# Optimization experiments

Hardware: AMD Instinct MI355X
Metric: run time of the kernel (lower is better)

Reference implementation:

```python
import jax, jax.numpy as jnp
import numpy as np

DIM, E_DIM, HID = 512, 1024, 256
N_EXP, N_MIC, TOP_K, TOP_K_MIC = 8, 325, 2, 8
EPS_LN = 1e-5


def _layernorm(x, g, b):
    mu = x.mean(-1, keepdims=True)
    var = ((x - mu) ** 2).mean(-1, keepdims=True)
    return (x - mu) / jnp.sqrt(var + EPS_LN) * g + b


def setup_inputs() -> dict:
    key = jax.random.key(0)
    ks = jax.random.split(key, 20)
    s = 0.02
    return {
        "x": jax.random.normal(ks[0], (2, 512, DIM), jnp.float32),
        "router_w": jax.random.normal(ks[1], (N_EXP, DIM), jnp.float32) * s,
        "router_b": jnp.zeros((N_EXP,), jnp.float32),
        "exp_w1": jax.random.normal(ks[2], (N_EXP, E_DIM, DIM), jnp.float32) * s,
        "exp_b1": jnp.zeros((N_EXP, E_DIM), jnp.float32),
        "exp_w2": jax.random.normal(ks[3], (N_EXP, DIM, E_DIM), jnp.float32) * s,
        "exp_b2": jnp.zeros((N_EXP, DIM), jnp.float32),
        "mrouter_w": jax.random.normal(ks[4], (N_MIC, DIM), jnp.float32) * s,
        "mrouter_b": jnp.zeros((N_MIC,), jnp.float32),
        "mic_w1": jax.random.normal(ks[5], (N_MIC, HID, DIM), jnp.float32) * s,
        "mic_b1": jnp.zeros((N_MIC, HID), jnp.float32),
        "mic_w2": jax.random.normal(ks[6], (N_MIC, DIM, HID), jnp.float32) * s,
        "mic_b2": jnp.zeros((N_MIC, DIM), jnp.float32),
        "mic_g": jnp.ones((N_MIC, DIM), jnp.float32),
        "mic_beta": jnp.zeros((N_MIC, DIM), jnp.float32),
        "norm_g": jnp.ones((DIM,), jnp.float32),
        "norm_b": jnp.zeros((DIM,), jnp.float32),
    }


def _forward(x, router_w, router_b, exp_w1, exp_b1, exp_w2, exp_b2,
             mrouter_w, mrouter_b, mic_w1, mic_b1, mic_w2, mic_b2,
             mic_g, mic_beta, norm_g, norm_b):
    B, S, D = x.shape
    xf = x.reshape(-1, D)  # [T, D]

    # ---- expert routing (top-2 of 8) ----
    probs = jax.nn.softmax(xf @ router_w.T + router_b, axis=-1)
    topp, topi = jax.lax.top_k(probs, TOP_K)
    topp = topp / (topp.sum(-1, keepdims=True) + 1e-8)

    # dense compute over 8 experts, combine with top-k weights
    h = jax.nn.gelu(jnp.einsum('td,ehd->teh', xf, exp_w1) + exp_b1, approximate=False)
    ye = jnp.einsum('teh,edh->ted', h, exp_w2) + exp_b2  # [T, E, D]
    comb_w = (jax.nn.one_hot(topi, N_EXP, dtype=xf.dtype) * topp[..., None]).sum(1)  # [T, E]
    eo = jnp.einsum('te,ted->td', comb_w, ye)

    # ---- micro routing (top-8 of 325) ----
    mprobs = jax.nn.softmax(eo @ mrouter_w.T + mrouter_b, axis=-1)
    mtopp, mtopi = jax.lax.top_k(mprobs, TOP_K_MIC)
    mtopp = mtopp / (mtopp.sum(-1, keepdims=True) + 1e-8)

    def micro_slot(eo, p, idx):
        # gather per-token micro params, batched GEMV dispatch
        hm = jax.nn.gelu(jnp.einsum('td,thd->th', eo, mic_w1[idx]) + mic_b1[idx],
                         approximate=False)
        ym = jnp.einsum('th,tdh->td', hm, mic_w2[idx]) + mic_b2[idx]
        n = _layernorm(eo + ym, mic_g[idx], mic_beta[idx])
        return p[:, None] * n

    micro_slot = jax.checkpoint(micro_slot, static_argnums=())
    mo = jnp.zeros_like(eo)
    for k in range(TOP_K_MIC):  # small fixed loop over slots
        mo = mo + micro_slot(eo, mtopp[:, k], mtopi[:, k])

    combined = (eo + 0.1 * mo).reshape(B, S, D)
    return _layernorm(combined, norm_g, norm_b)


def reference(x, router_w, router_b, exp_w1, exp_b1, exp_w2, exp_b2,
              mrouter_w, mrouter_b, mic_w1, mic_b1, mic_w2, mic_b2,
              mic_g, mic_beta, norm_g, norm_b):
    return _forward(x, router_w, router_b, exp_w1, exp_b1, exp_w2, exp_b2,
                    mrouter_w, mrouter_b, mic_w1, mic_b1, mic_w2, mic_b2,
                    mic_g, mic_beta, norm_g, norm_b)
```

## Files before the change

### kernel.cpp

```cpp
#include <hip/hip_runtime.h>
#include <hip/hip_bf16.h>
#include <math.h>

#define T_TOK 1024
#define DIMM  512
#define EDIM  1024
#define HIDD  256
#define NEXP  8
#define NMIC  325
#define E16TILES 136
#define MTILES  840
#define NPAIR_M 8192

typedef __attribute__((ext_vector_type(8))) short bf16x8;
typedef __attribute__((ext_vector_type(8))) _Float16 f16x8;
typedef __attribute__((ext_vector_type(4))) float f32x4;

__device__ __forceinline__ float dot4(float4 a, float4 b) {
    return a.x*b.x + a.y*b.y + a.z*b.z + a.w*b.w;
}
__device__ __forceinline__ float gelu_exact(float x) {
    return 0.5f * x * (1.0f + erff(x * 0.70710678118654752f));
}
__device__ __forceinline__ float wave_sum(float v) {
    #pragma unroll
    for (int o = 32; o; o >>= 1) v += __shfl_xor(v, o);
    return v;
}
__device__ __forceinline__ short f2bf(float f) {
    union { __hip_bfloat16 h; short s; } u;
    u.h = __float2bfloat16(f);
    return u.s;
}
__device__ __forceinline__ short f2h(float f) {
    union { _Float16 h; short s; } u;
    u.h = (_Float16)f;
    return u.s;
}
__device__ __forceinline__ float h2f(short s) {
    union { _Float16 h; short s; } u;
    u.s = s;
    return (float)u.h;
}

__global__ void k_router(const float* __restrict__ x, const float* __restrict__ rw,
                         const float* __restrict__ rb, int* __restrict__ eidx,
                         float* __restrict__ ew, int* __restrict__ ecnt) {
    int wave = threadIdx.x >> 6, lane = threadIdx.x & 63;
    int t = blockIdx.x * 4 + wave;
    if (t >= T_TOK) return;
    const float* xr = x + (size_t)t * DIMM;
    float xv[8];
    #pragma unroll
    for (int j = 0; j < 8; ++j) xv[j] = xr[lane + 64*j];
    float p[NEXP];
    #pragma unroll
    for (int e = 0; e < NEXP; ++e) {
        const float* wr = rw + (size_t)e * DIMM;
        float a = 0.f;
        #pragma unroll
        for (int j = 0; j < 8; ++j) a += xv[j] * wr[lane + 64*j];
        p[e] = wave_sum(a) + rb[e];
    }
    float m = p[0];
    #pragma unroll
    for (int e = 1; e < NEXP; ++e) m = fmaxf(m, p[e]);
    float Z = 0.f;
    #pragma unroll
    for (int e = 0; e < NEXP; ++e) { p[e] = expf(p[e] - m); Z += p[e]; }
    #pragma unroll
    for (int e = 0; e < NEXP; ++e) p[e] /= Z;
    int i1 = 0; float v1 = p[0];
    #pragma unroll
    for (int e = 1; e < NEXP; ++e) if (p[e] > v1) { v1 = p[e]; i1 = e; }
    int i2 = -1; float v2 = -1.f;
    #pragma unroll
    for (int e = 0; e < NEXP; ++e) if (e != i1 && p[e] > v2) { v2 = p[e]; i2 = e; }
    float s = v1 + v2 + 1e-8f;
    if (lane == 0) {
        eidx[t*2] = i1; eidx[t*2+1] = i2;
        ew[t*2] = v1 / s; ew[t*2+1] = v2 / s;
        atomicAdd(&ecnt[i1], 1); atomicAdd(&ecnt[i2], 1);
    }
}

__global__ void k_scan(const int* __restrict__ cnt, int n, int pm,
                       int* __restrict__ off, int* __restrict__ cur,
                       int2* __restrict__ tiles, int* __restrict__ ntile) {
    __shared__ int s[512], s2[512];
    int tid = threadIdx.x;
    int v  = (tid < n) ? cnt[tid] : 0;
    int tc = (v + pm - 1) / pm;
    s[tid] = v; s2[tid] = tc;
    __syncthreads();
    for (int d = 1; d < 512; d <<= 1) {
        int a = (tid >= d) ? s[tid-d] : 0;
        int b = (tid >= d) ? s2[tid-d] : 0;
        __syncthreads();
        s[tid] += a; s2[tid] += b;
        __syncthreads();
    }
    int myoff = s[tid] - v, tb = s2[tid] - tc;
    if (tid < n) { off[tid] = myoff; cur[tid] = myoff; }
    if (tid == n-1) off[n] = s[tid];
    if (tid == 511) *ntile = s2[511];
    for (int j = 0; j < tc; ++j) tiles[tb + j] = make_int2(tid, myoff + j*pm);
}

__global__ void k_scatter(const int* __restrict__ idx, const float* __restrict__ w,
                          int total, int S, int* __restrict__ cur,
                          int* __restrict__ ptok, float* __restrict__ pw,
                          int* __restrict__ pmi) {
    int g = blockIdx.x * blockDim.x + threadIdx.x;
    if (g >= total) return;
    int t = g / S;
    int e = idx[g];
    int pos = atomicAdd(&cur[e], 1);
    ptok[pos] = t; pw[pos] = w[g]; pmi[pos] = e;
}

__global__ __launch_bounds__(256) void k_wsplit(const float* __restrict__ w,
                                                short* __restrict__ hi,
                                                short* __restrict__ lo, int n4) {
    int g = blockIdx.x * blockDim.x + threadIdx.x;
    if (g >= n4) return;
    float4 v = ((const float4*)w)[g];
    short4 h4, l4;
    h4.x = f2h(v.x); l4.x = f2h((v.x - h2f(h4.x)) * 4096.f);
    h4.y = f2h(v.y); l4.y = f2h((v.y - h2f(h4.y)) * 4096.f);
    h4.z = f2h(v.z); l4.z = f2h((v.z - h2f(h4.z)) * 4096.f);
    h4.w = f2h(v.w); l4.w = f2h((v.w - h2f(h4.w)) * 4096.f);
    ((short4*)hi)[g] = h4;
    ((short4*)lo)[g] = l4;
}

__global__ __launch_bounds__(256) void k_effn1(
    const float* __restrict__ x, const short* __restrict__ w1h, const short* __restrict__ w1l,
    const float* __restrict__ b1,
    const int2* __restrict__ tiles, const int* __restrict__ ntile,
    const int* __restrict__ eoff, const int* __restrict__ ep_tok,
    short* __restrict__ ghhi, short* __restrict__ ghlo) {
    if ((int)blockIdx.x >= *ntile) return;
    int2 tl = tiles[blockIdx.x];
    int e = tl.x, pbase = tl.y;
    int m = min(16, eoff[e+1] - pbase);
    int by = blockIdx.y;
    __shared__ __align__(16) short xh[8192];
    __shared__ __align__(16) short xl[8192];
    __shared__ int tok_s[16];
    int tid = threadIdx.x;
    if (tid < 16) tok_s[tid] = ep_tok[pbase + ((tid < m) ? tid : 0)];
    __syncthreads();
    int m0 = tid & 15;
    const float4* xrow = (const float4*)(x + (size_t)tok_s[m0] * DIMM);
    for (int kk = tid >> 4; kk < 128; kk += 16) {
        float4 v = xrow[kk];
        int off = ((kk >> 3) * 512) + ((((kk >> 1) & 3) * 16 + m0) * 8) + ((kk & 1) * 4);
        short4 h4, l4;
        h4.x = f2h(v.x); l4.x = f2h((v.x - h2f(h4.x)) * 4096.f);
        h4.y = f2h(v.y); l4.y = f2h((v.y - h2f(h4.y)) * 4096.f);
        h4.z = f2h(v.z); l4.z = f2h((v.z - h2f(h4.z)) * 4096.f);
        h4.w = f2h(v.w); l4.w = f2h((v.w - h2f(h4.w)) * 4096.f);
        *(short4*)(xh + off) = h4;
        *(short4*)(xl + off) = l4;
    }
    __syncthreads();
    int wave = tid >> 6, lane = tid & 63;
    int quad = lane >> 4, lcol = lane & 15;
    f32x4 zero = {0.f, 0.f, 0.f, 0.f};
    f32x4 acc0[8], acc1[8];
    #pragma unroll
    for (int q = 0; q < 8; ++q) { acc0[q] = zero; acc1[q] = zero; }
    const short* w1hb = w1h + (size_t)e * EDIM * DIMM;
    const short* w1lb = w1l + (size_t)e * EDIM * DIMM;
    for (int ks = 0; ks < 16; ++ks) {
        f16x8 ah = *(const f16x8*)(xh + ks*512 + lane*8);
        f16x8 al = *(const f16x8*)(xl + ks*512 + lane*8);
        int kb = ks*32 + quad*8;
        #pragma unroll
        for (int q = 0; q < 8; ++q) {
            int n = by*512 + wave*128 + q*16 + lcol;
            size_t wo = (size_t)n * DIMM + kb;
            f16x8 wh = *(const f16x8*)(w1hb + wo);
            f16x8 wl = *(const f16x8*)(w1lb + wo);
            acc0[q] = __builtin_amdgcn_mfma_f32_16x16x32_f16(ah, wh, acc0[q], 0, 0, 0);
            acc1[q] = __builtin_amdgcn_mfma_f32_16x16x32_f16(al, wh, acc1[q], 0, 0, 0);
            acc1[q] = __builtin_amdgcn_mfma_f32_16x16x32_f16(ah, wl, acc1[q], 0, 0, 0);
        }
    }
    __syncthreads();
    #pragma unroll
    for (int q = 0; q < 8; ++q) {
        int hp = wave*128 + q*16 + lcol;
        float bb = b1[(size_t)e * EDIM + by*512 + hp];
        int obase = ((hp >> 5) * 512) + (((hp >> 3) & 3) * 16) * 8 + (hp & 7);
        #pragma unroll
        for (int r = 0; r < 4; ++r) {
            int mm = quad*4 + r;
            float hv = gelu_exact(acc0[q][r] + acc1[q][r] * (1.f/4096.f) + bb);
            short hh = f2h(hv);
            xh[obase + mm*8] = hh;
            xl[obase + mm*8] = f2h((hv - h2f(hh)) * 4096.f);
        }
    }
    __syncthreads();
    short* dh = ghhi + (size_t)blockIdx.x * 16384 + (size_t)by * 8192;
    short* dl = ghlo + (size_t)blockIdx.x * 16384 + (size_t)by * 8192;
    const int4* sh = (const int4*)xh;
    const int4* sl = (const int4*)xl;
    #pragma unroll
    for (int j = 0; j < 4; ++j) {
        ((int4*)dh)[tid + 256*j] = sh[tid + 256*j];
        ((int4*)dl)[tid + 256*j] = sl[tid + 256*j];
    }
}

__global__ __launch_bounds__(256) void k_effn2(
    const short* __restrict__ ghhi, const short* __restrict__ ghlo,
    const short* __restrict__ w2h, const short* __restrict__ w2l, const float* __restrict__ b2,
    const int2* __restrict__ tiles, const int* __restrict__ ntile,
    const int* __restrict__ eoff, const int* __restrict__ ep_tok, const float* __restrict__ ep_w,
    float* __restrict__ eo) {
    if ((int)blockIdx.x >= *ntile) return;
    int2 tl = tiles[blockIdx.x];
    int e = tl.x, pbase = tl.y;
    int m = min(16, eoff[e+1] - pbase);
    int by = blockIdx.y;
    __shared__ int tok_s[16];
    __shared__ float pw_s[16];
    int tid = threadIdx.x;
    if (tid < 16) {
        int ok = tid < m;
        tok_s[tid] = ok ? ep_tok[pbase + tid] : 0;
        pw_s[tid]  = ok ? ep_w[pbase + tid] : 0.f;
    }
    __syncthreads();
    int wave = tid >> 6, lane = tid & 63;
    int quad = lane >> 4, lcol = lane & 15;
    const short* ahb = ghhi + (size_t)blockIdx.x * 16384;
    const short* alb = ghlo + (size_t)blockIdx.x * 16384;
    f32x4 zero = {0.f, 0.f, 0.f, 0.f};
    f32x4 acc0[4], acc1[4];
    #pragma unroll
    for (int q = 0; q < 4; ++q) { acc0[q] = zero; acc1[q] = zero; }
    const short* w2hb = w2h + (size_t)e * DIMM * EDIM;
    const short* w2lb = w2l + (size_t)e * DIMM * EDIM;
    for (int ks = 0; ks < 32; ++ks) {
        f16x8 ah = *(const f16x8*)(ahb + ks*512 + lane*8);
        f16x8 al = *(const f16x8*)(alb + ks*512 + lane*8);
        int kb = ks*32 + quad*8;
        #pragma unroll
        for (int q = 0; q < 4; ++q) {
            int d = by*256 + wave*64 + q*16 + lcol;
            size_t wo = (size_t)d * EDIM + kb;
            f16x8 wh = *(const f16x8*)(w2hb + wo);
            f16x8 wl = *(const f16x8*)(w2lb + wo);
            acc0[q] = __builtin_amdgcn_mfma_f32_16x16x32_f16(ah, wh, acc0[q], 0, 0, 0);
            acc1[q] = __builtin_amdgcn_mfma_f32_16x16x32_f16(al, wh, acc1[q], 0, 0, 0);
            acc1[q] = __builtin_amdgcn_mfma_f32_16x16x32_f16(ah, wl, acc1[q], 0, 0, 0);
        }
    }
    #pragma unroll
    for (int q = 0; q < 4; ++q) {
        int d = by*256 + wave*64 + q*16 + lcol;
        float bb = b2[(size_t)e * DIMM + d];
        #pragma unroll
        for (int r = 0; r < 4; ++r) {
            int mm = quad*4 + r;
            if (mm < m) {
                float val = (acc0[q][r] + acc1[q][r] * (1.f/4096.f) + bb) * pw_s[mm];
                atomicAdd(&eo[(size_t)tok_s[mm] * DIMM + d], val);
            }
        }
    }
}

__global__ __launch_bounds__(384) void k_mlog(
    const float* __restrict__ eo, const float* __restrict__ mw, const float* __restrict__ mb,
    float* __restrict__ mlog) {
    int t0 = blockIdx.x * 4;
    __shared__ float4 es[4][128];
    int tid = threadIdx.x;
    const float4* eo4 = (const float4*)eo;
    for (int q = tid; q < 4*128; q += 384) {
        int i = q >> 7, k = q & 127;
        es[i][k] = eo4[(size_t)(t0 + i) * 128 + k];
    }
    __syncthreads();
    if (tid < NMIC) {
        const float4* wr = (const float4*)(mw + (size_t)tid * DIMM);
        float acc[4] = {0.f, 0.f, 0.f, 0.f};
        for (int kk = 0; kk < 128; ++kk) {
            float4 wv = wr[kk];
            #pragma unroll
            for (int i = 0; i < 4; ++i) acc[i] += dot4(wv, es[i][kk]);
        }
        float bb = mb[tid];
        #pragma unroll
        for (int i = 0; i < 4; ++i) mlog[(size_t)(t0 + i) * NMIC + tid] = acc[i] + bb;
    }
}

__global__ void k_mtop(const float* __restrict__ mlog, int* __restrict__ mtopi,
                       float* __restrict__ mtopp, int* __restrict__ mcnt) {
    int wave = threadIdx.x >> 6, lane = threadIdx.x & 63;
    int t = blockIdx.x * 4 + wave;
    if (t >= T_TOK) return;
    float v[6]; int vi[6];
    #pragma unroll
    for (int j = 0; j < 6; ++j) {
        int n = lane + 64*j;
        vi[j] = n;
        v[j] = (n < NMIC) ? mlog[(size_t)t * NMIC + n] : -1e30f;
    }
    float M = v[0];
    #pragma unroll
    for (int j = 1; j < 6; ++j) M = fmaxf(M, v[j]);
    #pragma unroll
    for (int o = 32; o; o >>= 1) M = fmaxf(M, __shfl_xor(M, o));
    float Z = 0.f;
    #pragma unroll
    for (int j = 0; j < 6; ++j) Z += expf(v[j] - M);
    Z = wave_sum(Z);
    float bk[8]; int bi[8];
    for (int k = 0; k < 8; ++k) {
        float lv = v[0]; int li = vi[0];
        #pragma unroll
        for (int j = 1; j < 6; ++j)
            if (v[j] > lv) { lv = v[j]; li = vi[j]; }
        #pragma unroll
        for (int o = 32; o; o >>= 1) {
            float ov = __shfl_xor(lv, o); int oi = __shfl_xor(li, o);
            if (ov > lv || (ov == lv && oi < li)) { lv = ov; li = oi; }
        }
        bk[k] = expf(lv - M) / Z; bi[k] = li;
        #pragma unroll
        for (int j = 0; j < 6; ++j) if (vi[j] == li) v[j] = -1e30f;
    }
    float s = 0.f;
    #pragma unroll
    for (int k = 0; k < 8; ++k) s += bk[k];
    s += 1e-8f;
    if (lane == 0) {
        for (int k = 0; k < 8; ++k) {
            mtopi[t*8 + k] = bi[k];
            mtopp[t*8 + k] = bk[k] / s;
            atomicAdd(&mcnt[bi[k]], 1);
        }
    }
}

__global__ __launch_bounds__(256) void k_mffn1(
    const float* __restrict__ eo, const float* __restrict__ w1, const float* __restrict__ b1,
    const int2* __restrict__ tiles, const int* __restrict__ ntile,
    const int* __restrict__ moff, const int* __restrict__ mp_tok,
    short* __restrict__ ghbuf) {
    if ((int)blockIdx.x >= *ntile) return;
    int2 tl = tiles[blockIdx.x];
    int mi = tl.x, pbase = tl.y;
    int pm = min(16, moff[mi+1] - pbase);
    int by = blockIdx.y;
    __shared__ __align__(16) short eof[8192];
    __shared__ __align__(16) short hf[2048];
    __shared__ int tok_s[16];
    int tid = threadIdx.x;
    if (tid < 16) tok_s[tid] = mp_tok[pbase + ((tid < pm) ? tid : 0)];
    __syncthreads();
    int m0 = tid & 15;
    const float4* eorow = (const float4*)(eo + (size_t)tok_s[m0] * DIMM);
    for (int kk = tid >> 4; kk < 128; kk += 16) {
        float4 v = eorow[kk];
        int off = ((kk >> 3) * 512) + ((((kk >> 1) & 3) * 16 + m0) * 8) + ((kk & 1) * 4);
        short4 s4; s4.x = f2bf(v.x); s4.y = f2bf(v.y); s4.z = f2bf(v.z); s4.w = f2bf(v.w);
        *(short4*)(eof + off) = s4;
    }
    __syncthreads();
    int wave = tid >> 6, lane = tid & 63;
    int quad = lane >> 4, lcol = lane & 15;
    f32x4 zero = {0.f, 0.f, 0.f, 0.f};
    f32x4 accA[2];
    accA[0] = zero; accA[1] = zero;
    const float* w1base = w1 + (size_t)mi * HIDD * DIMM;
    for (int ks = 0; ks < 16; ++ks) {
        bf16x8 a = *(bf16x8*)(eof + ks*512 + lane*8);
        int kb = ks*32 + quad*8;
        #pragma unroll
        for (int q = 0; q < 2; ++q) {
            int n = by*128 + wave*32 + q*16 + lcol;
            const float* wp = w1base + (size_t)n * DIMM + kb;
            float4 wa = *(const float4*)wp;
            float4 wb = *(const float4*)(wp + 4);
            bf16x8 bfr;
            bfr[0]=f2bf(wa.x); bfr[1]=f2bf(wa.y); bfr[2]=f2bf(wa.z); bfr[3]=f2bf(wa.w);
            bfr[4]=f2bf(wb.x); bfr[5]=f2bf(wb.y); bfr[6]=f2bf(wb.z); bfr[7]=f2bf(wb.w);
            accA[q] = __builtin_amdgcn_mfma_f32_16x16x32_bf16(a, bfr, accA[q], 0, 0, 0);
        }
    }
    #pragma unroll
    for (int q = 0; q < 2; ++q) {
        int hp = wave*32 + q*16 + lcol;
        float bb = b1[(size_t)mi * HIDD + by*128 + hp];
        int obase = ((hp >> 5) * 512) + (((hp >> 3) & 3) * 16) * 8 + (hp & 7);
        #pragma unroll
        for (int r = 0; r < 4; ++r) {
            int mm = quad*4 + r;
            hf[obase + mm*8] = f2bf(gelu_exact(accA[q][r] + bb));
        }
    }
    __syncthreads();
    short* gh = ghbuf + (size_t)blockIdx.x * 4096 + (size_t)by * 2048;
    ((int4*)gh)[tid] = ((const int4*)hf)[tid];
}

__global__ __launch_bounds__(256) void k_mffn2(
    const short* __restrict__ ghbuf, const float* __restrict__ w2, const float* __restrict__ b2,
    const int2* __restrict__ tiles, const int* __restrict__ ntile, const int* __restrict__ moff,
    float* __restrict__ ybuf) {
    if ((int)blockIdx.x >= *ntile) return;
    int2 tl = tiles[blockIdx.x];
    int mi = tl.x, pbase = tl.y;
    int pm = min(16, moff[mi+1] - pbase);
    int by = blockIdx.y;
    int tid = threadIdx.x, wave = tid >> 6, lane = tid & 63;
    int quad = lane >> 4, lcol = lane & 15;
    const short* gh = ghbuf + (size_t)blockIdx.x * 4096;
    f32x4 zero = {0.f, 0.f, 0.f, 0.f};
    f32x4 accB[4];
    #pragma unroll
    for (int q = 0; q < 4; ++q) accB[q] = zero;
    const float* w2base = w2 + (size_t)mi * DIMM * HIDD;
    for (int ks = 0; ks < 8; ++ks) {
        bf16x8 a = *(const bf16x8*)(gh + ks*512 + lane*8);
        int kb = ks*32 + quad*8;
        #pragma unroll
        for (int q = 0; q < 4; ++q) {
            int d = by*256 + wave*64 + q*16 + lcol;
            const float* wp = w2base + (size_t)d * HIDD + kb;
            float4 wa = *(const float4*)wp;
            float4 wb = *(const float4*)(wp + 4);
            bf16x8 bfr;
            bfr[0]=f2bf(wa.x); bfr[1]=f2bf(wa.y); bfr[2]=f2bf(wa.z); bfr[3]=f2bf(wa.w);
            bfr[4]=f2bf(wb.x); bfr[5]=f2bf(wb.y); bfr[6]=f2bf(wb.z); bfr[7]=f2bf(wb.w);
            accB[q] = __builtin_amdgcn_mfma_f32_16x16x32_bf16(a, bfr, accB[q], 0, 0, 0);
        }
    }
    #pragma unroll
    for (int q = 0; q < 4; ++q) {
        int d = by*256 + wave*64 + q*16 + lcol;
        float bb = b2[(size_t)mi * DIMM + d];
        #pragma unroll
        for (int r = 0; r < 4; ++r) {
            int mm = quad*4 + r;
            if (mm < pm) ybuf[(size_t)(pbase + mm) * DIMM + d] = accB[q][r] + bb;
        }
    }
}

__global__ __launch_bounds__(256) void k_mln(
    const float* __restrict__ ybuf, const float* __restrict__ eo,
    const float* __restrict__ g, const float* __restrict__ beta,
    const int* __restrict__ mp_tok, const float* __restrict__ mp_w,
    const int* __restrict__ mp_mi, float* __restrict__ mo) {
    int wave = threadIdx.x >> 6, lane = threadIdx.x & 63;
    int p = blockIdx.x * 4 + wave;
    int t = mp_tok[p];
    int mi = mp_mi[p];
    float pw = mp_w[p];
    const float* yr = ybuf + (size_t)p * DIMM;
    const float* er = eo + (size_t)t * DIMM;
    float vv[8];
    float sum = 0.f;
    #pragma unroll
    for (int j = 0; j < 8; ++j) {
        int d = lane + 64*j;
        vv[j] = yr[d] + er[d];
        sum += vv[j];
    }
    sum = wave_sum(sum);
    float mu = sum * (1.f/512.f);
    float var = 0.f;
    #pragma unroll
    for (int j = 0; j < 8; ++j) { float d0 = vv[j] - mu; var += d0*d0; }
    var = wave_sum(var) * (1.f/512.f);
    float rstd = rsqrtf(var + 1e-5f);
    #pragma unroll
    for (int j = 0; j < 8; ++j) {
        int d = lane + 64*j;
        float nj = (vv[j] - mu) * rstd * g[(size_t)mi * DIMM + d] + beta[(size_t)mi * DIMM + d];
        atomicAdd(&mo[(size_t)t * DIMM + d], pw * nj);
    }
}

__global__ void k_final(const float* __restrict__ eo, const float* __restrict__ mo,
                        const float* __restrict__ g, const float* __restrict__ b,
                        float* __restrict__ out) {
    int wave = threadIdx.x >> 6, lane = threadIdx.x & 63;
    int t = blockIdx.x * 4 + wave;
    if (t >= T_TOK) return;
    float vv[8];
    float sum = 0.f;
    #pragma unroll
    for (int j = 0; j < 8; ++j) {
        int d = lane + 64*j;
        vv[j] = eo[(size_t)t * DIMM + d] + 0.1f * mo[(size_t)t * DIMM + d];
        sum += vv[j];
    }
    sum = wave_sum(sum);
    float mu = sum * (1.f/512.f);
    float var = 0.f;
    #pragma unroll
    for (int j = 0; j < 8; ++j) { float d0 = vv[j] - mu; var += d0*d0; }
    var = wave_sum(var) * (1.f/512.f);
    float rstd = rsqrtf(var + 1e-5f);
    #pragma unroll
    for (int j = 0; j < 8; ++j) {
        int d = lane + 64*j;
        out[(size_t)t * DIMM + d] = (vv[j] - mu) * rstd * g[d] + b[d];
    }
}

extern "C" void kernel_launch(void* const* d_in, const int* in_sizes, int n_in,
                              void* d_out, int out_size, void* d_ws, size_t ws_size,
                              hipStream_t stream) {
    const float* x    = (const float*)d_in[0];
    const float* rw   = (const float*)d_in[1];
    const float* rb   = (const float*)d_in[2];
    const float* ew1  = (const float*)d_in[3];
    const float* eb1  = (const float*)d_in[4];
    const float* ew2  = (const float*)d_in[5];
    const float* eb2  = (const float*)d_in[6];
    const float* mrw  = (const float*)d_in[7];
    const float* mrb  = (const float*)d_in[8];
    const float* mw1  = (const float*)d_in[9];
    const float* mb1  = (const float*)d_in[10];
    const float* mw2  = (const float*)d_in[11];
    const float* mb2  = (const float*)d_in[12];
    const float* mg   = (const float*)d_in[13];
    const float* mbeta= (const float*)d_in[14];
    const float* ng   = (const float*)d_in[15];
    const float* nb   = (const float*)d_in[16];
    float* out = (float*)d_out;

    char* w = (char*)d_ws;
    auto alloc = [&](size_t bytes) -> char* {
        char* p = w;
        w += (bytes + 255) & ~(size_t)255;
        return p;
    };
    const size_t WELEM = (size_t)NEXP * EDIM * DIMM;
    float* eo    = (float*)alloc((size_t)T_TOK * DIMM * 4);
    float* mo    = (float*)alloc((size_t)T_TOK * DIMM * 4);
    short* wspl  = (short*)alloc(WELEM * 2 * 4);
    short* w1h   = wspl;
    short* w1l   = wspl + WELEM;
    short* w2h   = wspl + 2*WELEM;
    short* w2l   = wspl + 3*WELEM;
    float* ybuf  = (float*)wspl;
    short* gfrag = (short*)alloc((size_t)E16TILES * 16384 * 2 * 2);
    short* ehhi  = gfrag;
    short* ehlo  = gfrag + (size_t)E16TILES * 16384;
    short* ghbuf = gfrag;
    float* mlog  = (float*)alloc((size_t)T_TOK * NMIC * 4);
    float* ewts  = (float*)alloc(2048 * 4);
    float* mtopp = (float*)alloc(8192 * 4);
    float* ep_w  = (float*)alloc(2048 * 4);
    float* mp_w  = (float*)alloc(8192 * 4);
    int*   eidx  = (int*)alloc(2048 * 4);
    int*   mtopi = (int*)alloc(8192 * 4);
    int*   cnts  = (int*)alloc((NEXP + NMIC) * 4);
    int*   ecnt  = cnts;
    int*   mcnt  = cnts + NEXP;
    int*   eoff  = (int*)alloc((NEXP + 1) * 4);
    int*   ecur  = (int*)alloc(NEXP * 4);
    int*   moff  = (int*)alloc((NMIC + 1) * 4);
    int*   mcur  = (int*)alloc(NMIC * 4);
    int2*  etile = (int2*)alloc(E16TILES * 8);
    int2*  mtile = (int2*)alloc(MTILES * 8);
    int*   entile= (int*)alloc(4);
    int*   mntile= (int*)alloc(4);
    int*   ep_tok= (int*)alloc(2048 * 4);
    int*   mp_tok= (int*)alloc(8192 * 4);
    int*   ep_mi = (int*)alloc(2048 * 4);
    int*   mp_mi = (int*)alloc(8192 * 4);

    hipMemsetAsync(eo, 0, (size_t)2 * T_TOK * DIMM * 4, stream);
    hipMemsetAsync(cnts, 0, (NEXP + NMIC) * 4, stream);

    int n4 = (int)(WELEM / 4);
    k_wsplit <<<n4/256, 256, 0, stream>>>(ew1, w1h, w1l, n4);
    k_wsplit <<<n4/256, 256, 0, stream>>>(ew2, w2h, w2l, n4);
    k_router <<<T_TOK/4, 256, 0, stream>>>(x, rw, rb, eidx, ewts, ecnt);
    k_scan   <<<1, 512, 0, stream>>>(ecnt, NEXP, 16, eoff, ecur, etile, entile);
    k_scatter<<<(T_TOK*2 + 255)/256, 256, 0, stream>>>(eidx, ewts, T_TOK*2, 2, ecur, ep_tok, ep_w, ep_mi);
    k_effn1  <<<dim3(E16TILES, 2, 1), 256, 0, stream>>>(x, w1h, w1l, eb1, etile, entile, eoff, ep_tok, ehhi, ehlo);
    k_effn2  <<<dim3(E16TILES, 2, 1), 256, 0, stream>>>(ehhi, ehlo, w2h, w2l, eb2, etile, entile, eoff, ep_tok, ep_w, eo);
    k_mlog   <<<T_TOK/4, 384, 0, stream>>>(eo, mrw, mrb, mlog);
    k_mtop   <<<T_TOK/4, 256, 0, stream>>>(mlog, mtopi, mtopp, mcnt);
    k_scan   <<<1, 512, 0, stream>>>(mcnt, NMIC, 16, moff, mcur, mtile, mntile);
    k_scatter<<<(T_TOK*8 + 255)/256, 256, 0, stream>>>(mtopi, mtopp, T_TOK*8, 8, mcur, mp_tok, mp_w, mp_mi);
    k_mffn1  <<<dim3(MTILES, 2, 1), 256, 0, stream>>>(eo, mw1, mb1, mtile, mntile, moff, mp_tok, ghbuf);
    k_mffn2  <<<dim3(MTILES, 2, 1), 256, 0, stream>>>(ghbuf, mw2, mb2, mtile, mntile, moff, ybuf);
    k_mln    <<<NPAIR_M/4, 256, 0, stream>>>(ybuf, eo, mg, mbeta, mp_tok, mp_w, mp_mi, mo);
    k_final  <<<T_TOK/4, 256, 0, stream>>>(eo, mo, ng, nb, out);
}
```

Baseline: 697.9 us.

## Pre-pack expert and micro-expert weights into MFMA fragment layout

```diff
diff --git a/kernel.cpp b/kernel.cpp
--- a/kernel.cpp
+++ b/kernel.cpp
@@ -41,6 +41,63 @@
     union { _Float16 h; short s; } u;
     u.s = s;
     return (float)u.h;
+}
+
+__global__ __launch_bounds__(256) void k_packbf(const float* __restrict__ src,
+                                                short* __restrict__ dst,
+                                                int K, int CK, int nchunk) {
+    int c = blockIdx.x;
+    int rt = c / nchunk, kc = c - rt * nchunk;
+    __shared__ __align__(16) short lds[8192];
+    int tid = threadIdx.x;
+    const float4* s4 = (const float4*)(src + (size_t)rt * 16 * K + (size_t)kc * CK);
+    int ck4 = CK >> 2;
+    int tot = 16 * ck4;
+    for (int q = tid; q < tot; q += 256) {
+        int i = q / ck4, kk = q - i * ck4;
+        float4 v = s4[(size_t)i * (K >> 2) + kk];
+        int off = ((kk >> 3) * 512) + ((((kk >> 1) & 3) * 16 + i) * 8) + ((kk & 1) * 4);
+        short4 b4; b4.x = f2bf(v.x); b4.y = f2bf(v.y); b4.z = f2bf(v.z); b4.w = f2bf(v.w);
+        *(short4*)(lds + off) = b4;
+    }
+    __syncthreads();
+    short* d = dst + (size_t)rt * 16 * K + (size_t)kc * 16 * CK;
+    int n16 = (16 * CK) >> 3;
+    for (int q = tid; q < n16; q += 256)
+        ((int4*)d)[q] = ((const int4*)lds)[q];
+}
+
+__global__ __launch_bounds__(256) void k_packhl(const float* __restrict__ src,
+                                                short* __restrict__ dsth,
+                                                short* __restrict__ dstl,
+                                                int K, int CK, int nchunk) {
+    int c = blockIdx.x;
+    int rt = c / nchunk, kc = c - rt * nchunk;
+    __shared__ __align__(16) short ldh[8192];
+    __shared__ __align__(16) short ldl[8192];
+    int tid = threadIdx.x;
+    const float4* s4 = (const float4*)(src + (size_t)rt * 16 * K + (size_t)kc * CK);
+    int ck4 = CK >> 2;
+    int tot = 16 * ck4;
+    for (int q = tid; q < tot; q += 256) {
+        int i = q / ck4, kk = q - i * ck4;
+        float4 v = s4[(size_t)i * (K >> 2) + kk];
+        int off = ((kk >> 3) * 512) + ((((kk >> 1) & 3) * 16 + i) * 8) + ((kk & 1) * 4);
+        short4 h4, l4;
+        h4.x = f2h(v.x); l4.x = f2h((v.x - h2f(h4.x)) * 4096.f);
+        h4.y = f2h(v.y); l4.y = f2h((v.y - h2f(h4.y)) * 4096.f);
+        h4.z = f2h(v.z); l4.z = f2h((v.z - h2f(h4.z)) * 4096.f);
+        h4.w = f2h(v.w); l4.w = f2h((v.w - h2f(h4.w)) * 4096.f);
+        *(short4*)(ldh + off) = h4;
+        *(short4*)(ldl + off) = l4;
+    }
+    __syncthreads();
+    size_t cb = (size_t)rt * 16 * K + (size_t)kc * 16 * CK;
+    int n16 = (16 * CK) >> 3;
+    for (int q = tid; q < n16; q += 256) {
+        ((int4*)(dsth + cb))[q] = ((const int4*)ldh)[q];
+        ((int4*)(dstl + cb))[q] = ((const int4*)ldl)[q];
+    }
 }
 
 __global__ void k_router(const float* __restrict__ x, const float* __restrict__ rw,
@@ -117,21 +174,6 @@
     int e = idx[g];
     int pos = atomicAdd(&cur[e], 1);
     ptok[pos] = t; pw[pos] = w[g]; pmi[pos] = e;
-}
-
-__global__ __launch_bounds__(256) void k_wsplit(const float* __restrict__ w,
-                                                short* __restrict__ hi,
-                                                short* __restrict__ lo, int n4) {
-    int g = blockIdx.x * blockDim.x + threadIdx.x;
-    if (g >= n4) return;
-    float4 v = ((const float4*)w)[g];
-    short4 h4, l4;
-    h4.x = f2h(v.x); l4.x = f2h((v.x - h2f(h4.x)) * 4096.f);
-    h4.y = f2h(v.y); l4.y = f2h((v.y - h2f(h4.y)) * 4096.f);
-    h4.z = f2h(v.z); l4.z = f2h((v.z - h2f(h4.z)) * 4096.f);
-    h4.w = f2h(v.w); l4.w = f2h((v.w - h2f(h4.w)) * 4096.f);
-    ((short4*)hi)[g] = h4;
-    ((short4*)lo)[g] = l4;
 }
 
 __global__ __launch_bounds__(256) void k_effn1(
@@ -171,18 +213,17 @@
     f32x4 acc0[8], acc1[8];
     #pragma unroll
     for (int q = 0; q < 8; ++q) { acc0[q] = zero; acc1[q] = zero; }
-    const short* w1hb = w1h + (size_t)e * EDIM * DIMM;
-    const short* w1lb = w1l + (size_t)e * EDIM * DIMM;
+    const short* whb = w1h + (size_t)e * EDIM * DIMM + (size_t)lane * 8;
+    const short* wlb = w1l + (size_t)e * EDIM * DIMM + (size_t)lane * 8;
     for (int ks = 0; ks < 16; ++ks) {
         f16x8 ah = *(const f16x8*)(xh + ks*512 + lane*8);
         f16x8 al = *(const f16x8*)(xl + ks*512 + lane*8);
-        int kb = ks*32 + quad*8;
         #pragma unroll
         for (int q = 0; q < 8; ++q) {
-            int n = by*512 + wave*128 + q*16 + lcol;
-            size_t wo = (size_t)n * DIMM + kb;
-            f16x8 wh = *(const f16x8*)(w1hb + wo);
-            f16x8 wl = *(const f16x8*)(w1lb + wo);
+            int nt = by*32 + wave*8 + q;
+            size_t fo = (size_t)(nt*16 + ks) * 512;
+            f16x8 wh = *(const f16x8*)(whb + fo);
+            f16x8 wl = *(const f16x8*)(wlb + fo);
             acc0[q] = __builtin_amdgcn_mfma_f32_16x16x32_f16(ah, wh, acc0[q], 0, 0, 0);
             acc1[q] = __builtin_amdgcn_mfma_f32_16x16x32_f16(al, wh, acc1[q], 0, 0, 0);
             acc1[q] = __builtin_amdgcn_mfma_f32_16x16x32_f16(ah, wl, acc1[q], 0, 0, 0);
@@ -237,24 +278,23 @@
     __syncthreads();
     int wave = tid >> 6, lane = tid & 63;
     int quad = lane >> 4, lcol = lane & 15;
-    const short* ahb = ghhi + (size_t)blockIdx.x * 16384;
-    const short* alb = ghlo + (size_t)blockIdx.x * 16384;
+    const short* ahb = ghhi + (size_t)blockIdx.x * 16384 + (size_t)lane * 8;
+    const short* alb = ghlo + (size_t)blockIdx.x * 16384 + (size_t)lane * 8;
     f32x4 zero = {0.f, 0.f, 0.f, 0.f};
     f32x4 acc0[4], acc1[4];
     #pragma unroll
     for (int q = 0; q < 4; ++q) { acc0[q] = zero; acc1[q] = zero; }
-    const short* w2hb = w2h + (size_t)e * DIMM * EDIM;
-    const short* w2lb = w2l + (size_t)e * DIMM * EDIM;
+    const short* whb = w2h + (size_t)e * DIMM * EDIM + (size_t)lane * 8;
+    const short* wlb = w2l + (size_t)e * DIMM * EDIM + (size_t)lane * 8;
     for (int ks = 0; ks < 32; ++ks) {
-        f16x8 ah = *(const f16x8*)(ahb + ks*512 + lane*8);
-        f16x8 al = *(const f16x8*)(alb + ks*512 + lane*8);
-        int kb = ks*32 + quad*8;
+        f16x8 ah = *(const f16x8*)(ahb + ks*512);
+        f16x8 al = *(const f16x8*)(alb + ks*512);
         #pragma unroll
         for (int q = 0; q < 4; ++q) {
-            int d = by*256 + wave*64 + q*16 + lcol;
-            size_t wo = (size_t)d * EDIM + kb;
-            f16x8 wh = *(const f16x8*)(w2hb + wo);
-            f16x8 wl = *(const f16x8*)(w2lb + wo);
+            int nt = by*16 + wave*4 + q;
+            size_t fo = (size_t)(nt*32 + ks) * 512;
+            f16x8 wh = *(const f16x8*)(whb + fo);
+            f16x8 wl = *(const f16x8*)(wlb + fo);
             acc0[q] = __builtin_amdgcn_mfma_f32_16x16x32_f16(ah, wh, acc0[q], 0, 0, 0);
             acc1[q] = __builtin_amdgcn_mfma_f32_16x16x32_f16(al, wh, acc1[q], 0, 0, 0);
             acc1[q] = __builtin_amdgcn_mfma_f32_16x16x32_f16(ah, wl, acc1[q], 0, 0, 0);
@@ -351,7 +391,7 @@
 }
 
 __global__ __launch_bounds__(256) void k_mffn1(
-    const float* __restrict__ eo, const float* __restrict__ w1, const float* __restrict__ b1,
+    const float* __restrict__ eo, const short* __restrict__ w1f, const float* __restrict__ b1,
     const int2* __restrict__ tiles, const int* __restrict__ ntile,
     const int* __restrict__ moff, const int* __restrict__ mp_tok,
     short* __restrict__ ghbuf) {
@@ -380,19 +420,13 @@
     f32x4 zero = {0.f, 0.f, 0.f, 0.f};
     f32x4 accA[2];
     accA[0] = zero; accA[1] = zero;
-    const float* w1base = w1 + (size_t)mi * HIDD * DIMM;
+    const short* wb = w1f + (size_t)mi * HIDD * DIMM + (size_t)lane * 8;
     for (int ks = 0; ks < 16; ++ks) {
         bf16x8 a = *(bf16x8*)(eof + ks*512 + lane*8);
-        int kb = ks*32 + quad*8;
         #pragma unroll
         for (int q = 0; q < 2; ++q) {
-            int n = by*128 + wave*32 + q*16 + lcol;
-            const float* wp = w1base + (size_t)n * DIMM + kb;
-            float4 wa = *(const float4*)wp;
-            float4 wb = *(const float4*)(wp + 4);
-            bf16x8 bfr;
-            bfr[0]=f2bf(wa.x); bfr[1]=f2bf(wa.y); bfr[2]=f2bf(wa.z); bfr[3]=f2bf(wa.w);
-            bfr[4]=f2bf(wb.x); bfr[5]=f2bf(wb.y); bfr[6]=f2bf(wb.z); bfr[7]=f2bf(wb.w);
+            int nt = by*8 + wave*2 + q;
+            bf16x8 bfr = *(const bf16x8*)(wb + (size_t)(nt*16 + ks) * 512);
             accA[q] = __builtin_amdgcn_mfma_f32_16x16x32_bf16(a, bfr, accA[q], 0, 0, 0);
         }
     }
@@ -413,7 +447,7 @@
 }
 
 __global__ __launch_bounds__(256) void k_mffn2(
-    const short* __restrict__ ghbuf, const float* __restrict__ w2, const float* __restrict__ b2,
+    const short* __restrict__ ghbuf, const short* __restrict__ w2f, const float* __restrict__ b2,
     const int2* __restrict__ tiles, const int* __restrict__ ntile, const int* __restrict__ moff,
     float* __restrict__ ybuf) {
     if ((int)blockIdx.x >= *ntile) return;
@@ -423,24 +457,18 @@
     int by = blockIdx.y;
     int tid = threadIdx.x, wave = tid >> 6, lane = tid & 63;
     int quad = lane >> 4, lcol = lane & 15;
-    const short* gh = ghbuf + (size_t)blockIdx.x * 4096;
+    const short* gh = ghbuf + (size_t)blockIdx.x * 4096 + (size_t)lane * 8;
     f32x4 zero = {0.f, 0.f, 0.f, 0.f};
     f32x4 accB[4];
     #pragma unroll
     for (int q = 0; q < 4; ++q) accB[q] = zero;
-    const float* w2base = w2 + (size_t)mi * DIMM * HIDD;
+    const short* wb = w2f + (size_t)mi * DIMM * HIDD + (size_t)lane * 8;
     for (int ks = 0; ks < 8; ++ks) {
-        bf16x8 a = *(const bf16x8*)(gh + ks*512 + lane*8);
-        int kb = ks*32 + quad*8;
+        bf16x8 a = *(const bf16x8*)(gh + ks*512);
         #pragma unroll
         for (int q = 0; q < 4; ++q) {
-            int d = by*256 + wave*64 + q*16 + lcol;
-            const float* wp = w2base + (size_t)d * HIDD + kb;
-            float4 wa = *(const float4*)wp;
-            float4 wb = *(const float4*)(wp + 4);
-            bf16x8 bfr;
-            bfr[0]=f2bf(wa.x); bfr[1]=f2bf(wa.y); bfr[2]=f2bf(wa.z); bfr[3]=f2bf(wa.w);
-            bfr[4]=f2bf(wb.x); bfr[5]=f2bf(wb.y); bfr[6]=f2bf(wb.z); bfr[7]=f2bf(wb.w);
+            int nt = by*16 + wave*4 + q;
+            bf16x8 bfr = *(const bf16x8*)(wb + (size_t)(nt*8 + ks) * 512);
             accB[q] = __builtin_amdgcn_mfma_f32_16x16x32_bf16(a, bfr, accB[q], 0, 0, 0);
         }
     }
@@ -548,14 +576,17 @@
         return p;
     };
     const size_t WELEM = (size_t)NEXP * EDIM * DIMM;
+    const size_t MELEM = (size_t)NMIC * HIDD * DIMM;
     float* eo    = (float*)alloc((size_t)T_TOK * DIMM * 4);
     float* mo    = (float*)alloc((size_t)T_TOK * DIMM * 4);
-    short* wspl  = (short*)alloc(WELEM * 2 * 4);
-    short* w1h   = wspl;
-    short* w1l   = wspl + WELEM;
-    short* w2h   = wspl + 2*WELEM;
-    short* w2l   = wspl + 3*WELEM;
-    float* ybuf  = (float*)wspl;
+    short* bufA  = (short*)alloc(WELEM * 2 * 2);
+    short* w1h   = bufA;
+    short* w1l   = bufA + WELEM;
+    float* ybuf  = (float*)bufA;
+    short* bufB  = (short*)alloc(MELEM * 2);
+    short* w2h   = bufB;
+    short* w2l   = bufB + WELEM;
+    short* mwf   = bufB;
     short* gfrag = (short*)alloc((size_t)E16TILES * 16384 * 2 * 2);
     short* ehhi  = gfrag;
     short* ehlo  = gfrag + (size_t)E16TILES * 16384;
@@ -586,9 +617,9 @@
     hipMemsetAsync(eo, 0, (size_t)2 * T_TOK * DIMM * 4, stream);
     hipMemsetAsync(cnts, 0, (NEXP + NMIC) * 4, stream);
 
-    int n4 = (int)(WELEM / 4);
-    k_wsplit <<<n4/256, 256, 0, stream>>>(ew1, w1h, w1l, n4);
-    k_wsplit <<<n4/256, 256, 0, stream>>>(ew2, w2h, w2l, n4);
+    k_packhl<<<512, 256, 0, stream>>>(ew1, w1h, w1l, 512, 512, 1);
+    k_packhl<<<512, 256, 0, stream>>>(ew2, w2h, w2l, 1024, 512, 2);
+
     k_router <<<T_TOK/4, 256, 0, stream>>>(x, rw, rb, eidx, ewts, ecnt);
     k_scan   <<<1, 512, 0, stream>>>(ecnt, NEXP, 16, eoff, ecur, etile, entile);
     k_scatter<<<(T_TOK*2 + 255)/256, 256, 0, stream>>>(eidx, ewts, T_TOK*2, 2, ecur, ep_tok, ep_w, ep_mi);
@@ -598,8 +629,10 @@
     k_mtop   <<<T_TOK/4, 256, 0, stream>>>(mlog, mtopi, mtopp, mcnt);
     k_scan   <<<1, 512, 0, stream>>>(mcnt, NMIC, 16, moff, mcur, mtile, mntile);
     k_scatter<<<(T_TOK*8 + 255)/256, 256, 0, stream>>>(mtopi, mtopp, T_TOK*8, 8, mcur, mp_tok, mp_w, mp_mi);
-    k_mffn1  <<<dim3(MTILES, 2, 1), 256, 0, stream>>>(eo, mw1, mb1, mtile, mntile, moff, mp_tok, ghbuf);
-    k_mffn2  <<<dim3(MTILES, 2, 1), 256, 0, stream>>>(ghbuf, mw2, mb2, mtile, mntile, moff, ybuf);
+    k_packbf <<<5200, 256, 0, stream>>>(mw1, mwf, 512, 512, 1);
+    k_mffn1  <<<dim3(MTILES, 2, 1), 256, 0, stream>>>(eo, mwf, mb1, mtile, mntile, moff, mp_tok, ghbuf);
+    k_packbf <<<10400, 256, 0, stream>>>(mw2, mwf, 256, 256, 1);
+    k_mffn2  <<<dim3(MTILES, 2, 1), 256, 0, stream>>>(ghbuf, mwf, mb2, mtile, mntile, moff, ybuf);
     k_mln    <<<NPAIR_M/4, 256, 0, stream>>>(ybuf, eo, mg, mbeta, mp_tok, mp_w, mp_mi, mo);
     k_final  <<<T_TOK/4, 256, 0, stream>>>(eo, mo, ng, nb, out);
 }
```

Measured after the change: 680.7 us. 1.03x faster.
